# Optimization experiments

Measured on AMD Instinct MI355X. Metric: run time of the kernel, lower is better.

## Reference

```python
import jax, jax.numpy as jnp
import numpy as np

B, D_IN, T = 8, 1024, 2048
K, D_CB = 8192, 8
COMMIT = 0.005
CB_LOSS_W = 1.0
EPS = 1e-12  # F.normalize eps


def _wn(v, g):
    # torch weight_norm(dim=0) on a 1x1 Conv1d: w = g * v / ||v|| per output row
    return g[:, None] * v / jnp.linalg.norm(v, axis=1, keepdims=True)


def _l2n(x):
    return x / jnp.maximum(jnp.linalg.norm(x, axis=-1, keepdims=True), EPS)


def setup_inputs() -> dict:
    key = jax.random.key(0)
    ks = jax.random.split(key, 8)
    return {
        "z": jax.random.normal(ks[0], (B, D_IN, T), dtype=jnp.float32),
        "in_v": jax.random.normal(ks[1], (D_CB, D_IN), dtype=jnp.float32) * 0.02,
        "in_g": jnp.ones((D_CB,), dtype=jnp.float32),
        "in_b": jnp.zeros((D_CB,), dtype=jnp.float32),
        "out_v": jax.random.normal(ks[2], (D_IN, D_CB), dtype=jnp.float32) * 0.02,
        "out_g": jnp.ones((D_IN,), dtype=jnp.float32),
        "out_b": jnp.zeros((D_IN,), dtype=jnp.float32),
        "codebook": jax.random.normal(ks[3], (K, D_CB), dtype=jnp.float32),
    }


def reference(z, in_v, in_g, in_b, out_v, out_g, out_b, codebook):
    sg = jax.lax.stop_gradient
    # in_project: weight-normed 1x1 conv == matmul over channel dim
    w_in = _wn(in_v, in_g)
    z_e = jnp.einsum('oi,bit->bot', w_in, z) + in_b[None, :, None]  # [B, D_CB, T]

    # decode_latents
    enc = jnp.transpose(z_e, (0, 2, 1)).reshape(-1, D_CB)  # (B*T, D_CB)
    enc_n = _l2n(enc)
    cb_n = _l2n(codebook)
    dist = (jnp.sum(enc_n**2, axis=1, keepdims=True)
            - 2.0 * enc_n @ cb_n.T
            + jnp.sum(cb_n**2, axis=1)[None, :])  # (B*T, K)
    indices = jnp.argmin(dist, axis=1).reshape(B, T)  # [B, T]
    z_q = jnp.transpose(codebook[indices], (0, 2, 1))  # [B, D_CB, T] (unnormalized codebook)

    # training losses (per-batch means over (d, t))
    commit_loss = jnp.mean((z_e - sg(z_q)) ** 2, axis=(1, 2)) * COMMIT
    codebook_loss = jnp.mean((z_q - sg(z_e)) ** 2, axis=(1, 2)) * CB_LOSS_W

    # straight-through estimator
    z_q_st = z_e + sg(z_q - z_e)

    # out_project
    w_out = _wn(out_v, out_g)
    z_q_out = jnp.einsum('od,bdt->bot', w_out, z_q_st) + out_b[None, :, None]  # [B, D_IN, T]
    return (z_q_out, commit_loss, codebook_loss, indices, z_e)
```

## Files before the change

### kernel.cpp

```cpp
#include <hip/hip_runtime.h>
#include <math.h>
#include <stdint.h>

#define BB    8
#define DIN   1024
#define TT    2048
#define KK    8192
#define DCB   8
#define NPOS  (BB*TT)
#define KCHUNKS 64
#define KCH     (KK/KCHUNKS)
#define MARGIN  6e-4f

#define OFF_ZQOUT  0
#define OFF_COMMIT 16777216
#define OFF_CBLOSS 16777224
#define OFF_IDX    16777232
#define OFF_ZE     16793616

typedef short s8v __attribute__((ext_vector_type(8)));
typedef float f4v __attribute__((ext_vector_type(4)));

__device__ __forceinline__ unsigned short f2bf(float f) {
    unsigned u = __float_as_uint(f);
    u += 0x7FFF + ((u >> 16) & 1);
    return (unsigned short)(u >> 16);
}
__device__ __forceinline__ float bf2f(unsigned short h) {
    return __uint_as_float(((unsigned)h) << 16);
}

__global__ __launch_bounds__(256) void k_prep(
    const float* __restrict__ in_v, const float* __restrict__ in_g,
    const float* __restrict__ out_v, const float* __restrict__ out_g,
    const float* __restrict__ cb,
    float* __restrict__ w_in_f, float* __restrict__ w_out_f,
    double* __restrict__ cb_n, double* __restrict__ s_k,
    unsigned short* __restrict__ cb16, float* __restrict__ skp_f,
    double* __restrict__ lacc)
{
    __shared__ double red[256];
    int tid = threadIdx.x;
    int blk = blockIdx.x;

    if (blk < 8) {
        if (blk == 0 && tid < 64) lacc[tid] = 0.0;
        int r = blk;
        double s = 0.0;
        for (int i = tid; i < DIN; i += 256) {
            double v = (double)in_v[r*DIN + i];
            s += v*v;
        }
        red[tid] = s; __syncthreads();
        for (int off = 128; off > 0; off >>= 1) {
            if (tid < off) red[tid] += red[tid+off];
            __syncthreads();
        }
        double scale = (double)in_g[r] / sqrt(red[0]);
        for (int i = tid; i < DIN; i += 256)
            w_in_f[i*DCB + r] = (float)(scale * (double)in_v[r*DIN + i]);
    } else if (blk < 12) {
        int o = (blk-8)*256 + tid;
        float vv[DCB];
        double s = 0.0;
        #pragma unroll
        for (int d = 0; d < DCB; ++d) {
            vv[d] = out_v[o*DCB + d];
            s += (double)vv[d]*(double)vv[d];
        }
        double scale = (double)out_g[o] / sqrt(s);
        #pragma unroll
        for (int d = 0; d < DCB; ++d)
            w_out_f[o*DCB + d] = (float)(scale * (double)vv[d]);
    } else {
        int k = (blk-12)*256 + tid;
        double v[DCB]; double s = 0.0;
        #pragma unroll
        for (int d = 0; d < DCB; ++d) {
            v[d] = (double)cb[k*DCB + d];
            s += v[d]*v[d];
        }
        double nrm = sqrt(s);
        if (nrm < 1e-12) nrm = 1e-12;
        double s2 = 0.0;
        #pragma unroll
        for (int d = 0; d < DCB; ++d) {
            double t = v[d] / nrm;
            cb_n[(size_t)k*DCB + d] = t;
            s2 += t*t;
            float cf = (float)t;
            unsigned short bh = f2bf(cf);
            unsigned short bl = f2bf(cf - bf2f(bh));
            cb16[(size_t)k*16 + d]     = bh;
            cb16[(size_t)k*16 + 8 + d] = bl;
        }
        s_k[k] = s2;
        skp_f[k] = (float)(s2 + 4.0);
    }
}

__global__ __launch_bounds__(256) void k_inproj(
    const float* __restrict__ z, const float* __restrict__ w_in_f,
    const float* __restrict__ in_b,
    float* __restrict__ ze_out, double* __restrict__ enc_n,
    double* __restrict__ q_s, unsigned short* __restrict__ enc16)
{
    __shared__ float sm[DIN*DCB];

    int tid = threadIdx.x;
    {
        const uint4* src = (const uint4*)w_in_f;
        uint4* dst = (uint4*)sm;
        #pragma unroll
        for (int x = 0; x < 8; ++x) dst[tid + 256*x] = src[tid + 256*x];
    }
    __syncthreads();

    int p = tid & 7;
    int q = tid >> 3;
    int pos0 = blockIdx.x*32;
    int b = pos0 >> 11, t0 = pos0 & (TT-1);

    const float* zp = z + ((size_t)b*DIN + q)*TT + t0 + p*4;

    float acc[DCB][4];
    #pragma unroll
    for (int o = 0; o < DCB; ++o)
        #pragma unroll
        for (int j = 0; j < 4; ++j) acc[o][j] = 0.f;

    #pragma unroll
    for (int ii = 0; ii < 32; ++ii) {
        f4v zv = *(const f4v*)(zp + (size_t)ii*32*TT);
        const f4v* wp = (const f4v*)(sm + (ii*32 + q)*DCB);
        f4v w0 = wp[0], w1 = wp[1];
        #pragma unroll
        for (int j = 0; j < 4; ++j) {
            acc[0][j] += w0[0]*zv[j];
            acc[1][j] += w0[1]*zv[j];
            acc[2][j] += w0[2]*zv[j];
            acc[3][j] += w0[3]*zv[j];
            acc[4][j] += w1[0]*zv[j];
            acc[5][j] += w1[1]*zv[j];
            acc[6][j] += w1[2]*zv[j];
            acc[7][j] += w1[3]*zv[j];
        }
    }

    #pragma unroll
    for (int o = 0; o < DCB; ++o)
        #pragma unroll
        for (int j = 0; j < 4; ++j) {
            float v = acc[o][j];
            v += __shfl_xor(v, 8, 64);
            v += __shfl_xor(v, 16, 64);
            v += __shfl_xor(v, 32, 64);
            acc[o][j] = v;
        }

    __syncthreads();
    int lane = tid & 63, wv = tid >> 6;
    if ((lane >> 3) == 0) {
        float* rp = sm + wv*256 + p*32;
        #pragma unroll
        for (int o = 0; o < DCB; ++o)
            #pragma unroll
            for (int j = 0; j < 4; ++j) rp[o*4 + j] = acc[o][j];
    }
    __syncthreads();

    int o2 = tid & 7, p32 = tid >> 3;
    double s = 0.0;
    #pragma unroll
    for (int w2 = 0; w2 < 4; ++w2)
        s += (double)sm[w2*256 + (p32 >> 2)*32 + o2*4 + (p32 & 3)];
    s += (double)in_b[o2];

    int pos = pos0 + p32;
    int b3 = pos >> 11, t3 = pos & (TT-1);
    ze_out[((size_t)b3*DCB + o2)*TT + t3] = (float)s;

    double n2 = s*s;
    n2 += __shfl_xor(n2, 1, 64);
    n2 += __shfl_xor(n2, 2, 64);
    n2 += __shfl_xor(n2, 4, 64);
    double nrm = sqrt(n2);
    if (nrm < 1e-12) nrm = 1e-12;
    double e = s / nrm;
    enc_n[(size_t)pos*DCB + o2] = e;
    double s2 = e*e;
    s2 += __shfl_xor(s2, 1, 64);
    s2 += __shfl_xor(s2, 2, 64);
    s2 += __shfl_xor(s2, 4, 64);
    if (o2 == 0) q_s[pos] = s2;

    float ef = (float)(-2.0 * e);
    unsigned short ah = f2bf(ef);
    unsigned short al = f2bf(ef - bf2f(ah));
    enc16[(size_t)pos*16 + o2]     = ah;
    enc16[(size_t)pos*16 + 8 + o2] = al;
}

#define SCR_QB 64
#define SCR_CB 8
__global__ __launch_bounds__(256) void k_screen(
    const unsigned short* __restrict__ enc16,
    const unsigned short* __restrict__ cb16,
    const float* __restrict__ skp_f,
    int* __restrict__ d1key)
{
    __shared__ unsigned short cbl[SCR_CB*KCH*16];
    __shared__ float skl[SCR_CB*KCH];
    int tid = threadIdx.x;
    int cg = blockIdx.y;

    {
        const uint4* src = (const uint4*)(cb16 + (size_t)cg*SCR_CB*KCH*16);
        uint4* dst = (uint4*)cbl;
        for (int x = tid; x < SCR_CB*KCH*2; x += 256) dst[x] = src[x];
        const float* ss = skp_f + cg*SCR_CB*KCH;
        for (int x = tid; x < SCR_CB*KCH; x += 256) skl[x] = ss[x];
    }
    __syncthreads();

    int lane = tid & 63;
    int wv   = tid >> 6;
    int col  = lane & 15, quad = lane >> 4;
    int qbase = blockIdx.x*SCR_QB + wv*16;

    s8v a;
    {
        const s8v* ap = (const s8v*)(enc16 + ((size_t)(qbase + col))*16 + (quad==1 ? 8 : 0));
        a = *ap;
        if (quad == 3) { s8v zz = {0,0,0,0,0,0,0,0}; a = zz; }
    }
    int bsel = (quad == 2) ? 1 : 0;

    for (int c2 = 0; c2 < SCR_CB; ++c2) {
        int d0 = 0x7F800000, d1r = 0x7F800000, d2r = 0x7F800000, d3r = 0x7F800000;
        const s8v* bp = (const s8v*)(cbl + c2*KCH*16);
        const float* sp = skl + c2*KCH;
        #pragma unroll
        for (int t = 0; t < 8; ++t) {
            int n = t*16 + col;
            s8v bfr = bp[n*2 + bsel];
            float sk = sp[n];
            f4v acc = {sk, sk, sk, sk};
            acc = __builtin_amdgcn_mfma_f32_16x16x32_bf16(a, bfr, acc, 0, 0, 0);
            d0  = min(d0,  (int)(__float_as_uint(acc.x) | (unsigned)n));
            d1r = min(d1r, (int)(__float_as_uint(acc.y) | (unsigned)n));
            d2r = min(d2r, (int)(__float_as_uint(acc.z) | (unsigned)n));
            d3r = min(d3r, (int)(__float_as_uint(acc.w) | (unsigned)n));
        }
        #pragma unroll
        for (int off = 1; off < 16; off <<= 1) {
            d0  = min(d0,  __shfl_xor(d0,  off, 64));
            d1r = min(d1r, __shfl_xor(d1r, off, 64));
            d2r = min(d2r, __shfl_xor(d2r, off, 64));
            d3r = min(d3r, __shfl_xor(d3r, off, 64));
        }
        if (col == 0) {
            int chunk = cg*SCR_CB + c2;
            int qrow  = qbase + quad*4;
            int* dst = d1key + (size_t)qrow*KCHUNKS + chunk;
            dst[0*KCHUNKS] = d0;
            dst[1*KCHUNKS] = d1r;
            dst[2*KCHUNKS] = d2r;
            dst[3*KCHUNKS] = d3r;
        }
    }
}

__global__ __launch_bounds__(256) void k_verify(
    const int* __restrict__ d1key,
    const double* __restrict__ enc_n, const double* __restrict__ q_s,
    const double* __restrict__ cb_n, const double* __restrict__ s_k,
    const float* __restrict__ cb, const float* __restrict__ ze,
    float* __restrict__ idx_f, int* __restrict__ idx_i,
    double* __restrict__ lacc)
{
    __shared__ double sred[4];
    int tid = threadIdx.x;
    int lane = tid & 63;
    int wv = tid >> 6;
    int pos = blockIdx.x*4 + wv;

    int myk = d1key[(size_t)pos*KCHUNKS + lane];
    int m = myk;
    #pragma unroll
    for (int off = 1; off < 64; off <<= 1) m = min(m, __shfl_xor(m, off, 64));
    float thr = __int_as_float(m & 0xFFFFFF80) + MARGIN;
    bool scan = __int_as_float(myk & 0xFFFFFF80) <= thr;
    unsigned long long mask = __ballot(scan);

    double e[DCB];
    #pragma unroll
    for (int d = 0; d < DCB; ++d) e[d] = enc_n[(size_t)pos*DCB + d];
    double qs = q_s[pos];

    double bd = 1e300; int bi = 0x7FFFFFFF;
    while (mask) {
        int c = __ffsll((long long)mask) - 1;
        mask &= mask - 1;
        #pragma unroll
        for (int r = 0; r < KCH/64; ++r) {
            int k = c*KCH + r*64 + lane;
            const double* cp = cb_n + (size_t)k*DCB;
            double dot = e[0]*cp[0] + e[1]*cp[1] + e[2]*cp[2] + e[3]*cp[3]
                       + e[4]*cp[4] + e[5]*cp[5] + e[6]*cp[6] + e[7]*cp[7];
            double dist = qs - 2.0*dot + s_k[k];
            if (dist < bd || (dist == bd && k < bi)) { bd = dist; bi = k; }
        }
    }
    #pragma unroll
    for (int off = 1; off < 64; off <<= 1) {
        double od = __shfl_xor(bd, off, 64);
        int    oi = __shfl_xor(bi, off, 64);
        if (od < bd || (od == bd && oi < bi)) { bd = od; bi = oi; }
    }
    if (lane == 0) {
        int b = pos >> 11, t = pos & (TT-1);
        idx_f[pos] = (float)bi;
        idx_i[pos] = bi;
        double ssum = 0.0;
        #pragma unroll
        for (int d = 0; d < DCB; ++d) {
            double zev = (double)ze[((size_t)b*DCB + d)*TT + t];
            double zqv = (double)cb[bi*DCB + d];
            double diff = zev - zqv;
            ssum += diff*diff;
        }
        sred[wv] = ssum;
    }
    __syncthreads();
    if (tid == 0) {
        double t4 = sred[0] + sred[1] + sred[2] + sred[3];
        int b = (blockIdx.x*4) >> 11;
        atomicAdd(&lacc[b*8 + (blockIdx.x & 7)], t4);
    }
}

__global__ __launch_bounds__(256) void k_out_proj(
    const float* __restrict__ cb, const float* __restrict__ ze,
    const int* __restrict__ idx_i, const float* __restrict__ w_out,
    const float* __restrict__ out_b, const double* __restrict__ lacc,
    float* __restrict__ commit_out, float* __restrict__ cbloss_out,
    float* __restrict__ zq_out)
{
    __shared__ float wl[64*DCB];
    __shared__ float bl[64];
    int tid = threadIdx.x;

    if (blockIdx.x == 0 && blockIdx.y == 0 && tid < 8) {
        double s = 0.0;
        #pragma unroll
        for (int j = 0; j < 8; ++j) s += lacc[tid*8 + j];
        double mm = s / (double)(DCB*TT);
        commit_out[tid] = (float)(mm * 0.005);
        cbloss_out[tid] = (float)mm;
    }

    int oc = blockIdx.y;
    int obase = oc*64;
    for (int x = tid; x < 64*DCB; x += 256) wl[x] = w_out[obase*DCB + x];
    if (tid < 64) bl[tid] = out_b[obase + tid];
    __syncthreads();

    int pos = blockIdx.x*256 + tid;
    int b = pos >> 11, t = pos & (TT-1);
    int ki = idx_i[pos];
    float zq[DCB];
    #pragma unroll
    for (int d = 0; d < DCB; ++d) {
        float zev = ze[((size_t)b*DCB + d)*TT + t];
        float zqv = cb[ki*DCB + d];
        zq[d] = zev + (zqv - zev);
    }
    float* outp = zq_out + ((size_t)b*DIN + obase)*TT + t;
    for (int oo = 0; oo < 64; ++oo) {
        float acc = 0.f;
        #pragma unroll
        for (int d = 0; d < DCB; ++d) acc += wl[oo*DCB + d]*zq[d];
        acc += bl[oo];
        outp[(size_t)oo*TT] = acc;
    }
}

extern "C" void kernel_launch(void* const* d_in, const int* in_sizes, int n_in,
                              void* d_out, int out_size, void* d_ws, size_t ws_size,
                              hipStream_t stream)
{
    const float* z        = (const float*)d_in[0];
    const float* in_v     = (const float*)d_in[1];
    const float* in_g     = (const float*)d_in[2];
    const float* in_b     = (const float*)d_in[3];
    const float* out_v    = (const float*)d_in[4];
    const float* out_g    = (const float*)d_in[5];
    const float* out_b    = (const float*)d_in[6];
    const float* codebook = (const float*)d_in[7];

    float* out = (float*)d_out;
    float* zq_out_p  = out + OFF_ZQOUT;
    float* commit_p  = out + OFF_COMMIT;
    float* cbloss_p  = out + OFF_CBLOSS;
    float* idx_p     = out + OFF_IDX;
    float* ze_p      = out + OFF_ZE;

    float*  w_in_f = (float*)d_ws;
    double* cb_n   = (double*)d_ws + DCB*DIN;
    double* s_k    = cb_n + (size_t)KK*DCB;
    double* enc_n  = s_k + KK;
    double* q_s    = enc_n + (size_t)NPOS*DCB;
    double* loss_q = q_s + NPOS;
    float*  w_out  = (float*)(loss_q + NPOS);
    float*  skp_f  = w_out + DCB*DIN;
    unsigned short* cb16  = (unsigned short*)(skp_f + KK);
    unsigned short* enc16 = cb16 + (size_t)KK*16;
    int*    d1key  = (int*)(enc16 + (size_t)NPOS*16);
    int*    idx_i  = d1key + (size_t)NPOS*KCHUNKS;
    double* lacc   = (double*)(idx_i + NPOS);

    k_prep<<<44, 256, 0, stream>>>(in_v, in_g, out_v, out_g, codebook,
                                   w_in_f, w_out, cb_n, s_k, cb16, skp_f, lacc);
    k_inproj<<<NPOS/32, 256, 0, stream>>>(z, w_in_f, in_b, ze_p, enc_n, q_s, enc16);
    k_screen<<<dim3(NPOS/SCR_QB, KCHUNKS/SCR_CB), 256, 0, stream>>>(
        enc16, cb16, skp_f, d1key);
    k_verify<<<NPOS/4, 256, 0, stream>>>(d1key, enc_n, q_s, cb_n, s_k,
                                         codebook, ze_p, idx_p, idx_i, lacc);
    k_out_proj<<<dim3(NPOS/256, DIN/64), 256, 0, stream>>>(
        codebook, ze_p, idx_i, w_out, out_b, lacc, commit_p, cbloss_p, zq_out_p);
}
```

Baseline: 190.4 us.

## Restructure screening MFMA to reuse codebook tiles across four query fragments

```diff
diff --git a/kernel.cpp b/kernel.cpp
--- a/kernel.cpp
+++ b/kernel.cpp
@@ -201,7 +201,6 @@
     enc16[(size_t)pos*16 + 8 + o2] = al;
 }
 
-#define SCR_QB 64
 #define SCR_CB 8
 __global__ __launch_bounds__(256) void k_screen(
     const unsigned short* __restrict__ enc16,
@@ -209,64 +208,66 @@
     const float* __restrict__ skp_f,
     int* __restrict__ d1key)
 {
-    __shared__ unsigned short cbl[SCR_CB*KCH*16];
+    __shared__ unsigned short cbh[SCR_CB*KCH*8];
+    __shared__ unsigned short cbl[SCR_CB*KCH*8];
     __shared__ float skl[SCR_CB*KCH];
     int tid = threadIdx.x;
     int cg = blockIdx.y;
 
     {
         const uint4* src = (const uint4*)(cb16 + (size_t)cg*SCR_CB*KCH*16);
-        uint4* dst = (uint4*)cbl;
-        for (int x = tid; x < SCR_CB*KCH*2; x += 256) dst[x] = src[x];
-        const float* ss = skp_f + cg*SCR_CB*KCH;
-        for (int x = tid; x < SCR_CB*KCH; x += 256) skl[x] = ss[x];
+        uint4* dh = (uint4*)cbh;
+        uint4* dl = (uint4*)cbl;
+        #pragma unroll
+        for (int x = 0; x < 4; ++x) {
+            int n = tid + 256*x;
+            dh[n] = src[2*n];
+            dl[n] = src[2*n + 1];
+        }
+        const float* ss = skp_f + (size_t)cg*SCR_CB*KCH;
+        #pragma unroll
+        for (int x = 0; x < 4; ++x) skl[tid + 256*x] = ss[tid + 256*x];
     }
     __syncthreads();
 
     int lane = tid & 63;
     int wv   = tid >> 6;
     int col  = lane & 15, quad = lane >> 4;
-    int qbase = blockIdx.x*SCR_QB + wv*16;
-
-    s8v a;
-    {
-        const s8v* ap = (const s8v*)(enc16 + ((size_t)(qbase + col))*16 + (quad==1 ? 8 : 0));
-        a = *ap;
-        if (quad == 3) { s8v zz = {0,0,0,0,0,0,0,0}; a = zz; }
-    }
-    int bsel = (quad == 2) ? 1 : 0;
+    int qbase = blockIdx.x*256 + wv*64;
+
+    s8v bfr[4];
+    #pragma unroll
+    for (int f = 0; f < 4; ++f)
+        bfr[f] = *(const s8v*)(enc16 + ((size_t)(qbase + f*16 + col))*16 + (quad >= 2 ? 8 : 0));
+
+    const unsigned short* aplane = (quad & 1) ? cbl : cbh;
 
     for (int c2 = 0; c2 < SCR_CB; ++c2) {
-        int d0 = 0x7F800000, d1r = 0x7F800000, d2r = 0x7F800000, d3r = 0x7F800000;
-        const s8v* bp = (const s8v*)(cbl + c2*KCH*16);
-        const float* sp = skl + c2*KCH;
+        float dmin0 = INFINITY, dmin1 = INFINITY, dmin2 = INFINITY, dmin3 = INFINITY;
         #pragma unroll
         for (int t = 0; t < 8; ++t) {
-            int n = t*16 + col;
-            s8v bfr = bp[n*2 + bsel];
-            float sk = sp[n];
-            f4v acc = {sk, sk, sk, sk};
-            acc = __builtin_amdgcn_mfma_f32_16x16x32_bf16(a, bfr, acc, 0, 0, 0);
-            d0  = min(d0,  (int)(__float_as_uint(acc.x) | (unsigned)n));
-            d1r = min(d1r, (int)(__float_as_uint(acc.y) | (unsigned)n));
-            d2r = min(d2r, (int)(__float_as_uint(acc.z) | (unsigned)n));
-            d3r = min(d3r, (int)(__float_as_uint(acc.w) | (unsigned)n));
-        }
-        #pragma unroll
-        for (int off = 1; off < 16; off <<= 1) {
-            d0  = min(d0,  __shfl_xor(d0,  off, 64));
-            d1r = min(d1r, __shfl_xor(d1r, off, 64));
-            d2r = min(d2r, __shfl_xor(d2r, off, 64));
-            d3r = min(d3r, __shfl_xor(d3r, off, 64));
-        }
-        if (col == 0) {
-            int chunk = cg*SCR_CB + c2;
-            int qrow  = qbase + quad*4;
-            int* dst = d1key + (size_t)qrow*KCHUNKS + chunk;
-            dst[0*KCHUNKS] = d0;
-            dst[1*KCHUNKS] = d1r;
-            dst[2*KCHUNKS] = d2r;
-            dst[3*KCHUNKS] = d3r;
+            int nb = c2*KCH + t*16;
+            s8v a = *(const s8v*)(aplane + (size_t)(nb + col)*8);
+            f4v sk4 = *(const f4v*)(skl + nb + quad*4);
+            f4v acc;
+            acc = __builtin_amdgcn_mfma_f32_16x16x32_bf16(a, bfr[0], sk4, 0, 0, 0);
+            dmin0 = fminf(dmin0, fminf(fminf(acc.x, acc.y), fminf(acc.z, acc.w)));
+            acc = __builtin_amdgcn_mfma_f32_16x16x32_bf16(a, bfr[1], sk4, 0, 0, 0);
+            dmin1 = fminf(dmin1, fminf(fminf(acc.x, acc.y), fminf(acc.z, acc.w)));
+            acc = __builtin_amdgcn_mfma_f32_16x16x32_bf16(a, bfr[2], sk4, 0, 0, 0);
+            dmin2 = fminf(dmin2, fminf(fminf(acc.x, acc.y), fminf(acc.z, acc.w)));
+            acc = __builtin_amdgcn_mfma_f32_16x16x32_bf16(a, bfr[3], sk4, 0, 0, 0);
+            dmin3 = fminf(dmin3, fminf(fminf(acc.x, acc.y), fminf(acc.z, acc.w)));
+        }
+        int chunk = cg*SCR_CB + c2;
+        float dm[4] = {dmin0, dmin1, dmin2, dmin3};
+        #pragma unroll
+        for (int f = 0; f < 4; ++f) {
+            float v = dm[f];
+            v = fminf(v, __shfl_xor(v, 16, 64));
+            v = fminf(v, __shfl_xor(v, 32, 64));
+            if (quad == 0)
+                d1key[(size_t)(qbase + f*16 + col)*KCHUNKS + chunk] = __float_as_int(v);
         }
     }
 }
@@ -347,8 +348,8 @@
     float* __restrict__ commit_out, float* __restrict__ cbloss_out,
     float* __restrict__ zq_out)
 {
-    __shared__ float wl[64*DCB];
-    __shared__ float bl[64];
+    __shared__ float wl[128*DCB];
+    __shared__ float bl[128];
     int tid = threadIdx.x;
 
     if (blockIdx.x == 0 && blockIdx.y == 0 && tid < 8) {
@@ -361,9 +362,9 @@
     }
 
     int oc = blockIdx.y;
-    int obase = oc*64;
-    for (int x = tid; x < 64*DCB; x += 256) wl[x] = w_out[obase*DCB + x];
-    if (tid < 64) bl[tid] = out_b[obase + tid];
+    int obase = oc*128;
+    for (int x = tid; x < 128*DCB; x += 256) wl[x] = w_out[obase*DCB + x];
+    for (int x = tid; x < 128; x += 256) bl[x] = out_b[obase + x];
     __syncthreads();
 
     int pos = blockIdx.x*256 + tid;
@@ -377,7 +378,7 @@
         zq[d] = zev + (zqv - zev);
     }
     float* outp = zq_out + ((size_t)b*DIN + obase)*TT + t;
-    for (int oo = 0; oo < 64; ++oo) {
+    for (int oo = 0; oo < 128; ++oo) {
         float acc = 0.f;
         #pragma unroll
         for (int d = 0; d < DCB; ++d) acc += wl[oo*DCB + d]*zq[d];
@@ -423,10 +424,10 @@
     k_prep<<<44, 256, 0, stream>>>(in_v, in_g, out_v, out_g, codebook,
                                    w_in_f, w_out, cb_n, s_k, cb16, skp_f, lacc);
     k_inproj<<<NPOS/32, 256, 0, stream>>>(z, w_in_f, in_b, ze_p, enc_n, q_s, enc16);
-    k_screen<<<dim3(NPOS/SCR_QB, KCHUNKS/SCR_CB), 256, 0, stream>>>(
+    k_screen<<<dim3(NPOS/256, KCHUNKS/SCR_CB), 256, 0, stream>>>(
         enc16, cb16, skp_f, d1key);
     k_verify<<<NPOS/4, 256, 0, stream>>>(d1key, enc_n, q_s, cb_n, s_k,
                                          codebook, ze_p, idx_p, idx_i, lacc);
-    k_out_proj<<<dim3(NPOS/256, DIN/64), 256, 0, stream>>>(
+    k_out_proj<<<dim3(NPOS/256, DIN/128), 256, 0, stream>>>(
         codebook, ze_p, idx_i, w_out, out_b, lacc, commit_p, cbloss_p, zq_out_p);
 }
```

Measured after the change: 180.0 us (median of 2 runs). 5.5% less time.
